# Kernel tuning notes

Hardware: AMD Instinct MI355X
Metric: run time of the kernel (lower is better)

Reference implementation:

```python
import jax, jax.numpy as jnp
import numpy as np

BN_EPS = 0.001
ALPHA = 10.0
WEIGHT_BIT = 8
ACT_BIT = 8
BIAS_BIT = 16


def _ste_round(x, s):
    # straight-through quantize: round(x*s)/s with identity gradient
    return x + jax.lax.stop_gradient(jnp.round(x * s) / s - x)


def _qsym(x, bit):
    # symmetric per-tensor 'scale' quantization
    s = (2.0 ** (bit - 1) - 1.0) / jnp.maximum(jnp.max(jnp.abs(x)), 1e-8)
    return _ste_round(x, s)


def _qrelu(x, alpha, bit):
    # clipped ReLU to [0, alpha] then uniform quantization to 2^bit - 1 levels
    y = jnp.clip(x, 0.0, alpha)
    s = (2.0 ** bit - 1.0) / alpha
    return _ste_round(y, s)


def _folded_qconv(x, w, b, gamma, beta, mean, var, stride, pad):
    # fold BN into conv weights/bias, then quantize weight (8b) and bias (16b)
    sc = gamma / jnp.sqrt(var + BN_EPS)            # [O]
    wf = _qsym(w * sc[:, None, None, None], WEIGHT_BIT)
    bf = _qsym((b - mean) * sc + beta, BIAS_BIT)
    y = jax.lax.conv_general_dilated(
        x, wf, window_strides=stride, padding=[(pad, pad), (pad, pad)],
        dimension_numbers=('NCHW', 'OIHW', 'NCHW'))
    return y + bf[None, :, None, None]


def setup_inputs() -> dict:
    key = jax.random.key(0)
    ks = jax.random.split(key, 20)
    Cin, Cmid, Cout = 256, 128, 512
    d = {'x': jax.random.normal(ks[0], (32, Cin, 56, 56), dtype=jnp.float32)}

    def mk(k0, o, i, kh, kw, tag):
        kk = jax.random.split(k0, 6)
        fan = i * kh * kw
        d['w' + tag] = jax.random.normal(kk[0], (o, i, kh, kw), jnp.float32) * (fan ** -0.5)
        d['b' + tag] = jax.random.normal(kk[1], (o,), jnp.float32) * 0.01
        d['g' + tag] = 1.0 + jax.random.normal(kk[2], (o,), jnp.float32) * 0.1
        d['be' + tag] = jax.random.normal(kk[3], (o,), jnp.float32) * 0.1
        d['m' + tag] = jax.random.normal(kk[4], (o,), jnp.float32) * 0.1
        d['v' + tag] = jax.random.uniform(kk[5], (o,), jnp.float32) + 0.5

    mk(ks[1], Cmid, Cin, 1, 1, '1')
    mk(ks[2], Cmid, Cmid, 3, 3, '2')
    mk(ks[3], Cout, Cmid, 1, 1, '3')
    return d


def reference(x, w1, b1, g1, be1, m1, v1,
              w2, b2, g2, be2, m2, v2,
              w3, b3, g3, be3, m3, v3):
    out = _folded_qconv(x, w1, b1, g1, be1, m1, v1, (1, 1), 0)
    out = _qrelu(out, ALPHA, ACT_BIT)
    out = _folded_qconv(out, w2, b2, g2, be2, m2, v2, (1, 1), 1)
    out = _qrelu(out, ALPHA, ACT_BIT)
    out = _folded_qconv(out, w3, b3, g3, be3, m3, v3, (1, 1), 0)
    return out
```

## Files before the change

### kernel.cpp

```cpp
#include <hip/hip_runtime.h>
#include <math.h>

typedef int v4i  __attribute__((ext_vector_type(4)));
typedef int v16i __attribute__((ext_vector_type(16)));
typedef short v8s __attribute__((ext_vector_type(8)));
typedef float v16f __attribute__((ext_vector_type(16)));

#define N_IMG 32
#define CIN   256
#define CMID  128
#define COUT  512
#define HWP   3136
#define W58   58
#define PLANE_Q 3456
#define CBSTRIDE (PLANE_Q*16)
#define IMGSTRIDE (8*CBSTRIDE)
#define BSROW 248
#define GUARD 16384
#define BN_EPS_F 1e-3f
#define ALPHA_F  10.0f
#define ARELU_S  25.5f

#define OFF_WQ1   0
#define OFF_WF2   32768
#define OFF_WF3   180224
#define OFF_BQ1   245760
#define OFF_BQ2   245888
#define OFF_BQ3   246016
#define OFF_MAX   246528
#define OFF_Q2    246536
#define OFF_Q3    246664
#define OFF_WQ2I  247296
#define OFF_WQ3I  284160
#define OFF_WBF1  300544
#define ACT1Q_GUARD_B 52582400u
#define ACT1Q_B       (ACT1Q_GUARD_B + GUARD)
#define ACT2Q_B       (ACT1Q_B + (unsigned)(N_IMG*IMGSTRIDE) + GUARD)

__device__ __forceinline__ void async16(const char* g, char* l) {
    __builtin_amdgcn_global_load_lds((const __attribute__((address_space(1))) void*)g,
                                     (__attribute__((address_space(3))) void*)l, 16, 0, 0);
}

__device__ __forceinline__ unsigned bf16rne(float f) {
    unsigned u = __float_as_uint(f);
    return (u + 0x7fffu + ((u >> 16) & 1u)) >> 16;
}
__device__ __forceinline__ float bfval(unsigned h) {
    return __uint_as_float(h << 16);
}

__global__ __launch_bounds__(256) void fold_max_kernel(
    const float* __restrict__ w, const float* __restrict__ g,
    const float* __restrict__ v, float* __restrict__ wf,
    unsigned int* __restrict__ maxbits, int inner, int total)
{
    __shared__ float smax[256];
    float m = 0.f;
    for (int i = blockIdx.x * 256 + threadIdx.x; i < total; i += gridDim.x * 256) {
        int o = i / inner;
        float sc = g[o] / sqrtf(v[o] + BN_EPS_F);
        float val = w[i] * sc;
        wf[i] = val;
        m = fmaxf(m, fabsf(val));
    }
    smax[threadIdx.x] = m;
    __syncthreads();
    for (int s = 128; s > 0; s >>= 1) {
        if (threadIdx.x < s) smax[threadIdx.x] = fmaxf(smax[threadIdx.x], smax[threadIdx.x + s]);
        __syncthreads();
    }
    if (threadIdx.x == 0) atomicMax(maxbits, __float_as_uint(smax[0]));
}

__global__ __launch_bounds__(256) void quant_w1_bf16_kernel(
    const float* __restrict__ wf1, const unsigned int* __restrict__ maxbits,
    unsigned short* __restrict__ wbf)
{
    int i = blockIdx.x * 256 + threadIdx.x;
    float s = 127.0f / fmaxf(__uint_as_float(*maxbits), 1e-8f);
    int kb = i >> 10, rem = i & 1023;
    int m = rem >> 3, j = rem & 7;
    int c = kb * 8 + j;
    float k = rintf(wf1[m * CIN + c] * s);
    wbf[i] = (unsigned short)(__float_as_uint(k) >> 16);
}

__global__ __launch_bounds__(256) void quant_w2_kernel(
    const float* __restrict__ wf2, const unsigned int* __restrict__ maxw,
    char* __restrict__ wq2i, int* __restrict__ Q2)
{
    __shared__ int red[256];
    int m = blockIdx.x;
    float s = 127.0f / fmaxf(__uint_as_float(maxw[1]), 1e-8f);
    int sum = 0;
    for (int idx = threadIdx.x; idx < CMID * 9; idx += 256) {
        int c = idx / 9, tap = idx - c * 9;
        int q = (int)rintf(wf2[(size_t)m * (CMID * 9) + idx] * s);
        wq2i[(size_t)tap * (CMID * CMID) + m * CMID + c] = (char)q;
        sum += q;
    }
    red[threadIdx.x] = sum;
    __syncthreads();
    for (int st = 128; st > 0; st >>= 1) {
        if (threadIdx.x < st) red[threadIdx.x] += red[threadIdx.x + st];
        __syncthreads();
    }
    if (threadIdx.x == 0) Q2[m] = red[0];
}

__global__ __launch_bounds__(128) void quant_w3_kernel(
    const float* __restrict__ wf3, const unsigned int* __restrict__ maxw,
    char* __restrict__ wq3i, int* __restrict__ Q3)
{
    __shared__ int red[128];
    int m = blockIdx.x, c = threadIdx.x;
    float s = 127.0f / fmaxf(__uint_as_float(maxw[2]), 1e-8f);
    int q = (int)rintf(wf3[(size_t)m * CMID + c] * s);
    wq3i[(size_t)m * CMID + c] = (char)q;
    red[c] = q;
    __syncthreads();
    for (int st = 64; st > 0; st >>= 1) {
        if (c < st) red[c] += red[c + st];
        __syncthreads();
    }
    if (c == 0) Q3[m] = red[0];
}

__global__ __launch_bounds__(512) void fold_bias_kernel(
    const float* __restrict__ b, const float* __restrict__ g,
    const float* __restrict__ be, const float* __restrict__ m,
    const float* __restrict__ v, float* __restrict__ bq, int n)
{
    __shared__ float red[512];
    int t = threadIdx.x;
    float val = 0.f;
    if (t < n) {
        float sc = g[t] / sqrtf(v[t] + BN_EPS_F);
        val = (b[t] - m[t]) * sc + be[t];
    }
    red[t] = (t < n) ? fabsf(val) : 0.f;
    __syncthreads();
    for (int s = 256; s > 0; s >>= 1) {
        if (t < s) red[t] = fmaxf(red[t], red[t + s]);
        __syncthreads();
    }
    float mx = fmaxf(red[0], 1e-8f);
    float s = 32767.0f / mx;
    if (t < n) bq[t] = rintf(val * s) / s;
}

__global__ __launch_bounds__(256) void conv1_bf16_kernel(
    const float* __restrict__ X, const unsigned short* __restrict__ Wbf,
    const unsigned int* __restrict__ maxw, const float* __restrict__ bq1,
    char* __restrict__ act1q)
{
    __shared__ char lds[65536];
    char* As = lds;
    char* Bh = lds + 16384;
    char* Bm = lds + 32768;
    char* Bl = lds + 49152;
    const int tid = threadIdx.x;
    const int n  = blockIdx.z;
    const int q0 = blockIdx.x * 128;
    const int lane = tid & 63, wid = tid >> 6;
    const int lo = lane & 31, hi = lane >> 5;
    const int wm = wid >> 1, wn = wid & 1;
    const float* Xn = X + (size_t)n * CIN * HWP;

    v16f acc[2][2] = {};

    for (int kc = 0; kc < 4; kc++) {
        __syncthreads();
        const char* wsrc = (const char*)Wbf + kc * 16384;
#pragma unroll
        for (int i = 0; i < 4; i++)
            async16(wsrc + (i * 256 + tid) * 16, As + (i * 256 + tid) * 16);
#pragma unroll
        for (int i = 0; i < 4; i++) {
            int e = i * 256 + tid;
            int kb = e >> 7, qi = e & 127;
            int q = q0 + qi;
            int y = q / W58, xx = q - y * W58;
            int p = (y - 1) * 56 + (xx - 1);
            p = p < 0 ? 0 : (p > HWP - 1 ? HWP - 1 : p);
            const float* src = Xn + (size_t)(kc * 64 + kb * 8) * HWP + p;
            float v[8];
#pragma unroll
            for (int j = 0; j < 8; j++) v[j] = src[j * HWP];
            unsigned ph[4], pm_[4], pl[4];
#pragma unroll
            for (int jj = 0; jj < 4; jj++) {
                float a0 = v[2 * jj], a1 = v[2 * jj + 1];
                unsigned h0 = bf16rne(a0), h1 = bf16rne(a1);
                float r0 = a0 - bfval(h0), r1 = a1 - bfval(h1);
                unsigned m0_ = bf16rne(r0), m1_ = bf16rne(r1);
                float t0 = r0 - bfval(m0_), t1 = r1 - bfval(m1_);
                unsigned l0 = bf16rne(t0), l1 = bf16rne(t1);
                ph[jj]  = h0 | (h1 << 16);
                pm_[jj] = m0_ | (m1_ << 16);
                pl[jj]  = l0 | (l1 << 16);
            }
            int off = (kb * 128 + qi) * 16;
            *(uint4*)(Bh + off) = make_uint4(ph[0], ph[1], ph[2], ph[3]);
            *(uint4*)(Bm + off) = make_uint4(pm_[0], pm_[1], pm_[2], pm_[3]);
            *(uint4*)(Bl + off) = make_uint4(pl[0], pl[1], pl[2], pl[3]);
        }
        __syncthreads();
#pragma unroll
        for (int pass = 0; pass < 3; pass++) {
            const char* Bp = (pass == 0) ? Bh : ((pass == 1) ? Bm : Bl);
#pragma unroll
            for (int ks = 0; ks < 4; ks++) {
                v8s a[2], b[2];
#pragma unroll
                for (int s = 0; s < 2; s++)
                    a[s] = *(const v8s*)(As + ((ks * 2 + hi) * 128 + wm * 64 + s * 32 + lo) * 16);
#pragma unroll
                for (int t = 0; t < 2; t++)
                    b[t] = *(const v8s*)(Bp + ((ks * 2 + hi) * 128 + wn * 64 + t * 32 + lo) * 16);
#pragma unroll
                for (int s = 0; s < 2; s++)
#pragma unroll
                    for (int t = 0; t < 2; t++)
                        acc[s][t] = __builtin_amdgcn_mfma_f32_32x32x16_bf16(a[s], b[t], acc[s][t], 0, 0, 0);
            }
        }
    }

    float inv_s = fmaxf(__uint_as_float(maxw[0]), 1e-8f) / 127.0f;
    __syncthreads();
    char* Cs = lds;
#pragma unroll
    for (int s = 0; s < 2; s++)
#pragma unroll
        for (int t = 0; t < 2; t++) {
            int qloc = wn * 64 + t * 32 + lo;
#pragma unroll
            for (int reg = 0; reg < 16; reg++) {
                int m = wm * 64 + s * 32 + (reg & 3) + 8 * (reg >> 2) + 4 * hi;
                float val = fmaf(acc[s][t][reg], inv_s, bq1[m]);
                val = fminf(fmaxf(val, 0.f), ALPHA_F);
                int k1 = (int)rintf(val * ARELU_S);
                Cs[qloc * 148 + m] = (char)(k1 - 128);
            }
        }
    __syncthreads();
    char* dst = act1q + (size_t)n * IMGSTRIDE + (size_t)q0 * 16;
#pragma unroll
    for (int it = 0; it < 4; it++) {
        int idx = it * 256 + tid;
        int ql = idx >> 3, cb = idx & 7;
        int q = q0 + ql;
        int y = q / W58, xx = q - y * W58;
        if ((unsigned)(y - 1) < 56u && (unsigned)(xx - 1) < 56u) {
            int4 w;
            w.x = *(const int*)(Cs + ql * 148 + cb * 16 + 0);
            w.y = *(const int*)(Cs + ql * 148 + cb * 16 + 4);
            w.z = *(const int*)(Cs + ql * 148 + cb * 16 + 8);
            w.w = *(const int*)(Cs + ql * 148 + cb * 16 + 12);
            *(int4*)(dst + (size_t)cb * CBSTRIDE + ql * 16) = w;
        }
    }
}

__global__ __launch_bounds__(256) void conv2_i8_kernel(
    const char* __restrict__ actq, const char* __restrict__ wq2i,
    const int* __restrict__ Q2, const float* __restrict__ bq2,
    const unsigned int* __restrict__ maxw, char* __restrict__ act2q)
{
    __shared__ char lds[48128];
    char* As2 = lds;
    char* Bs  = lds + 16384;
    const int tid = threadIdx.x;
    const int n  = blockIdx.z;
    const int q0 = blockIdx.x * 128;
    const int lane = tid & 63, wid = tid >> 6;
    const int lo = lane & 31, hi = lane >> 5;
    const int wm = wid >> 1, wn = wid & 1;

    const char* src = actq + (size_t)n * IMGSTRIDE + (long)(q0 - 59) * 16;
#pragma unroll
    for (int cb = 0; cb < 8; cb++) {
        if (tid < 246)
            async16(src + (size_t)cb * CBSTRIDE + tid * 16, Bs + cb * (BSROW * 16) + tid * 16);
    }

    const int sm = tid >> 1, shalf = tid & 1;
    const char* wsrc = wq2i + sm * CMID + shalf * 64;
    char* wdst = As2 + (shalf * 4) * 2048 + sm * 16;
    int4 pre[4];
#pragma unroll
    for (int i = 0; i < 4; i++) pre[i] = *(const int4*)(wsrc + i * 16);

    v16i acc[2][2] = {};

    for (int tap = 0; tap < 9; tap++) {
        __syncthreads();
        int4 cur[4];
#pragma unroll
        for (int i = 0; i < 4; i++) cur[i] = pre[i];
        if (tap < 8) {
            const char* ns = wsrc + (size_t)(tap + 1) * (CMID * CMID);
#pragma unroll
            for (int i = 0; i < 4; i++) pre[i] = *(const int4*)(ns + i * 16);
        }
#pragma unroll
        for (int i = 0; i < 4; i++) *(int4*)(wdst + i * 2048) = cur[i];
        __syncthreads();

        const int tapoff = ((tap / 3) - 1) * W58 + (tap % 3) - 1;
#pragma unroll
        for (int ks = 0; ks < 4; ks++) {
            v4i a[2], b[2];
#pragma unroll
            for (int s = 0; s < 2; s++)
                a[s] = *(const v4i*)(As2 + ((ks * 2 + hi) * 128 + wm * 64 + s * 32 + lo) * 16);
#pragma unroll
            for (int t = 0; t < 2; t++) {
                int ql = 59 + tapoff + wn * 64 + t * 32 + lo;
                b[t] = *(const v4i*)(Bs + ((ks * 2 + hi) * BSROW + ql) * 16);
            }
#pragma unroll
            for (int s = 0; s < 2; s++)
#pragma unroll
                for (int t = 0; t < 2; t++)
                    acc[s][t] = __builtin_amdgcn_mfma_i32_32x32x32_i8(a[s], b[t], acc[s][t], 0, 0, 0);
        }
    }

    float scale = fmaxf(__uint_as_float(maxw[1]), 1e-8f) / (127.0f * ARELU_S);
    __syncthreads();
    char* Cs = lds;
#pragma unroll
    for (int s = 0; s < 2; s++)
#pragma unroll
        for (int t = 0; t < 2; t++) {
            int qloc = wn * 64 + t * 32 + lo;
#pragma unroll
            for (int reg = 0; reg < 16; reg++) {
                int m = wm * 64 + s * 32 + (reg & 3) + 8 * (reg >> 2) + 4 * hi;
                float val = fmaf((float)(acc[s][t][reg] + 128 * Q2[m]), scale, bq2[m]);
                val = fminf(fmaxf(val, 0.f), ALPHA_F);
                int k2 = (int)rintf(val * ARELU_S);
                Cs[qloc * 148 + m] = (char)(k2 - 128);
            }
        }
    __syncthreads();
    char* dst = act2q + (size_t)n * IMGSTRIDE + q0 * 16;
#pragma unroll
    for (int it = 0; it < 4; it++) {
        int idx = it * 256 + tid;
        int q = idx >> 3, cb = idx & 7;
        int4 w;
        w.x = *(const int*)(Cs + q * 148 + cb * 16 + 0);
        w.y = *(const int*)(Cs + q * 148 + cb * 16 + 4);
        w.z = *(const int*)(Cs + q * 148 + cb * 16 + 8);
        w.w = *(const int*)(Cs + q * 148 + cb * 16 + 12);
        *(int4*)(dst + (size_t)cb * CBSTRIDE + q * 16) = w;
    }
}

__global__ __launch_bounds__(256) void conv3_i8_kernel(
    const char* __restrict__ act2q, const char* __restrict__ wq3i,
    const int* __restrict__ Q3, const float* __restrict__ bq3,
    const unsigned int* __restrict__ maxw, float* __restrict__ out)
{
    __shared__ char lds[32768];
    char* As2 = lds;
    char* Bs  = lds + 16384;
    const int tid = threadIdx.x;
    const int n  = blockIdx.z;
    const int q0 = blockIdx.x * 128;
    const int m0 = blockIdx.y * 128;
    const int lane = tid & 63, wid = tid >> 6;
    const int lo = lane & 31, hi = lane >> 5;
    const int wm = wid >> 1, wn = wid & 1;

    const char* bsrc = act2q + (size_t)n * IMGSTRIDE + q0 * 16;
#pragma unroll
    for (int i = 0; i < 4; i++) {
        int cb = i * 2 + (tid >> 7), row = tid & 127;
        async16(bsrc + (size_t)cb * CBSTRIDE + row * 16, Bs + cb * 2048 + row * 16);
    }

    const int sm = tid >> 1, shalf = tid & 1;
    const char* wsrc = wq3i + (size_t)(m0 + sm) * CMID + shalf * 64;
    char* wdst = As2 + (shalf * 4) * 2048 + sm * 16;
    int4 w[4];
#pragma unroll
    for (int i = 0; i < 4; i++) w[i] = *(const int4*)(wsrc + i * 16);
#pragma unroll
    for (int i = 0; i < 4; i++) *(int4*)(wdst + i * 2048) = w[i];
    __syncthreads();

    v16i acc[2][2] = {};
#pragma unroll
    for (int ks = 0; ks < 4; ks++) {
        v4i a[2], b[2];
#pragma unroll
        for (int s = 0; s < 2; s++)
            a[s] = *(const v4i*)(As2 + ((ks * 2 + hi) * 128 + wm * 64 + s * 32 + lo) * 16);
#pragma unroll
        for (int t = 0; t < 2; t++)
            b[t] = *(const v4i*)(Bs + ((ks * 2 + hi) * 128 + wn * 64 + t * 32 + lo) * 16);
#pragma unroll
        for (int s = 0; s < 2; s++)
#pragma unroll
            for (int t = 0; t < 2; t++)
                acc[s][t] = __builtin_amdgcn_mfma_i32_32x32x32_i8(a[s], b[t], acc[s][t], 0, 0, 0);
    }

    float scale = fmaxf(__uint_as_float(maxw[2]), 1e-8f) / (127.0f * ARELU_S);
#pragma unroll
    for (int s = 0; s < 2; s++)
#pragma unroll
        for (int t = 0; t < 2; t++) {
            int q = q0 + wn * 64 + t * 32 + lo;
            int y = q / W58, x = q - y * W58;
            if ((unsigned)(y - 1) < 56u && (unsigned)(x - 1) < 56u) {
                int p = (y - 1) * 56 + (x - 1);
                float* op = out + (size_t)n * COUT * HWP + p;
#pragma unroll
                for (int reg = 0; reg < 16; reg++) {
                    int m = m0 + wm * 64 + s * 32 + (reg & 3) + 8 * (reg >> 2) + 4 * hi;
                    op[(size_t)m * HWP] = fmaf((float)(acc[s][t][reg] + 128 * Q3[m]), scale, bq3[m]);
                }
            }
        }
}

extern "C" void kernel_launch(void* const* d_in, const int* in_sizes, int n_in,
                              void* d_out, int out_size, void* d_ws, size_t ws_size,
                              hipStream_t stream) {
    const float* x   = (const float*)d_in[0];
    const float* w1  = (const float*)d_in[1];
    const float* b1  = (const float*)d_in[2];
    const float* g1  = (const float*)d_in[3];
    const float* be1 = (const float*)d_in[4];
    const float* m1  = (const float*)d_in[5];
    const float* v1  = (const float*)d_in[6];
    const float* w2  = (const float*)d_in[7];
    const float* b2  = (const float*)d_in[8];
    const float* g2  = (const float*)d_in[9];
    const float* be2 = (const float*)d_in[10];
    const float* m2  = (const float*)d_in[11];
    const float* v2  = (const float*)d_in[12];
    const float* w3  = (const float*)d_in[13];
    const float* b3  = (const float*)d_in[14];
    const float* g3  = (const float*)d_in[15];
    const float* be3 = (const float*)d_in[16];
    const float* m3  = (const float*)d_in[17];
    const float* v3  = (const float*)d_in[18];

    float* ws  = (float*)d_ws;
    unsigned char* wsb = (unsigned char*)d_ws;
    float* wq1 = ws + OFF_WQ1;
    float* wf2 = ws + OFF_WF2;
    float* wf3 = ws + OFF_WF3;
    float* bq1 = ws + OFF_BQ1;
    float* bq2 = ws + OFF_BQ2;
    float* bq3 = ws + OFF_BQ3;
    unsigned int* maxw = (unsigned int*)(ws + OFF_MAX);
    int* Q2 = (int*)(ws + OFF_Q2);
    int* Q3 = (int*)(ws + OFF_Q3);
    char* wq2i = (char*)(ws + OFF_WQ2I);
    char* wq3i = (char*)(ws + OFF_WQ3I);
    unsigned short* wbf = (unsigned short*)(ws + OFF_WBF1);
    char* act1q = (char*)(wsb + ACT1Q_B);
    char* act2q = (char*)(wsb + ACT2Q_B);
    float* out  = (float*)d_out;

    hipMemsetAsync(maxw, 0, 12, stream);
    hipMemsetAsync(wsb + ACT1Q_GUARD_B, 0x80, (size_t)GUARD + (size_t)N_IMG * IMGSTRIDE + GUARD, stream);

    fold_max_kernel<<<128, 256, 0, stream>>>(w1, g1, v1, wq1, maxw + 0, CIN,      CMID * CIN);
    fold_max_kernel<<<256, 256, 0, stream>>>(w2, g2, v2, wf2, maxw + 1, CMID * 9, CMID * CMID * 9);
    fold_max_kernel<<<256, 256, 0, stream>>>(w3, g3, v3, wf3, maxw + 2, CMID,     COUT * CMID);

    quant_w1_bf16_kernel<<<128, 256, 0, stream>>>(wq1, maxw + 0, wbf);
    quant_w2_kernel<<<CMID, 256, 0, stream>>>(wf2, maxw, wq2i, Q2);
    quant_w3_kernel<<<COUT, 128, 0, stream>>>(wf3, maxw, wq3i, Q3);

    fold_bias_kernel<<<1, 512, 0, stream>>>(b1, g1, be1, m1, v1, bq1, CMID);
    fold_bias_kernel<<<1, 512, 0, stream>>>(b2, g2, be2, m2, v2, bq2, CMID);
    fold_bias_kernel<<<1, 512, 0, stream>>>(b3, g3, be3, m3, v3, bq3, COUT);

    conv1_bf16_kernel<<<dim3(26, 1, 32), 256, 0, stream>>>(x, wbf, maxw, bq1, act1q);
    conv2_i8_kernel<<<dim3(27, 1, 32), 256, 0, stream>>>(act1q, wq2i, Q2, bq2, maxw, act2q);
    conv3_i8_kernel<<<dim3(27, 4, 32), 256, 0, stream>>>(act2q, wq3i, Q3, bq3, maxw, out);
}
```

Before: 521.6 us.

## Fuse prep kernels, read weights from global, vectorize conv1 input loads

Merges the nine weight/bias fold and quantize launches into two kernels. Drops the large border memset by having conv1 write the 0x80 padding value itself, with an extra grid column covering the tail. The conv kernels now read weight fragments straight from global memory in a pre-tiled layout instead of staging them in LDS, which shrinks LDS use. conv1 loads four pixels per thread with float4 when they are contiguous, and splits bf16 by truncation instead of round-to-nearest. These cut launch overhead, memset bandwidth and LDS traffic, but make weight reads depend on cache hits and change the rounding of the split.

```diff
diff --git a/kernel.cpp b/kernel.cpp
--- a/kernel.cpp
+++ b/kernel.cpp
@@ -42,112 +42,109 @@
                                      (__attribute__((address_space(3))) void*)l, 16, 0, 0);
 }
 
-__device__ __forceinline__ unsigned bf16rne(float f) {
-    unsigned u = __float_as_uint(f);
-    return (u + 0x7fffu + ((u >> 16) & 1u)) >> 16;
-}
-__device__ __forceinline__ float bfval(unsigned h) {
-    return __uint_as_float(h << 16);
-}
-
-__global__ __launch_bounds__(256) void fold_max_kernel(
-    const float* __restrict__ w, const float* __restrict__ g,
-    const float* __restrict__ v, float* __restrict__ wf,
-    unsigned int* __restrict__ maxbits, int inner, int total)
+__global__ __launch_bounds__(256) void fold_all_kernel(
+    const float* __restrict__ w1, const float* __restrict__ g1, const float* __restrict__ v1,
+    const float* __restrict__ w2, const float* __restrict__ g2, const float* __restrict__ v2,
+    const float* __restrict__ w3, const float* __restrict__ g3, const float* __restrict__ v3,
+    const float* __restrict__ b1, const float* __restrict__ be1, const float* __restrict__ m1,
+    const float* __restrict__ b2, const float* __restrict__ be2, const float* __restrict__ m2,
+    const float* __restrict__ b3, const float* __restrict__ be3, const float* __restrict__ m3,
+    float* __restrict__ wq1, float* __restrict__ wf2, float* __restrict__ wf3,
+    float* __restrict__ bq1, float* __restrict__ bq2, float* __restrict__ bq3,
+    unsigned int* __restrict__ maxw)
 {
-    __shared__ float smax[256];
-    float m = 0.f;
-    for (int i = blockIdx.x * 256 + threadIdx.x; i < total; i += gridDim.x * 256) {
+    __shared__ float red[256];
+    const int b = blockIdx.x, t = threadIdx.x;
+    if (b < 960) {
+        const float *w, *g, *v; float* wf; int inner; unsigned int* mslot; int i;
+        if (b < 128)      { w = w1; g = g1; v = v1; wf = wq1; inner = CIN;      mslot = maxw + 0; i = b * 256 + t; }
+        else if (b < 704) { w = w2; g = g2; v = v2; wf = wf2; inner = CMID * 9; mslot = maxw + 1; i = (b - 128) * 256 + t; }
+        else              { w = w3; g = g3; v = v3; wf = wf3; inner = CMID;     mslot = maxw + 2; i = (b - 704) * 256 + t; }
         int o = i / inner;
         float sc = g[o] / sqrtf(v[o] + BN_EPS_F);
         float val = w[i] * sc;
         wf[i] = val;
-        m = fmaxf(m, fabsf(val));
-    }
-    smax[threadIdx.x] = m;
-    __syncthreads();
-    for (int s = 128; s > 0; s >>= 1) {
-        if (threadIdx.x < s) smax[threadIdx.x] = fmaxf(smax[threadIdx.x], smax[threadIdx.x + s]);
-        __syncthreads();
-    }
-    if (threadIdx.x == 0) atomicMax(maxbits, __float_as_uint(smax[0]));
-}
-
-__global__ __launch_bounds__(256) void quant_w1_bf16_kernel(
-    const float* __restrict__ wf1, const unsigned int* __restrict__ maxbits,
-    unsigned short* __restrict__ wbf)
-{
-    int i = blockIdx.x * 256 + threadIdx.x;
-    float s = 127.0f / fmaxf(__uint_as_float(*maxbits), 1e-8f);
-    int kb = i >> 10, rem = i & 1023;
-    int m = rem >> 3, j = rem & 7;
-    int c = kb * 8 + j;
-    float k = rintf(wf1[m * CIN + c] * s);
-    wbf[i] = (unsigned short)(__float_as_uint(k) >> 16);
-}
-
-__global__ __launch_bounds__(256) void quant_w2_kernel(
-    const float* __restrict__ wf2, const unsigned int* __restrict__ maxw,
-    char* __restrict__ wq2i, int* __restrict__ Q2)
+        red[t] = fabsf(val);
+        __syncthreads();
+        for (int s = 128; s > 0; s >>= 1) {
+            if (t < s) red[t] = fmaxf(red[t], red[t + s]);
+            __syncthreads();
+        }
+        if (t == 0) atomicMax(mslot, __float_as_uint(red[0]));
+    } else {
+        const float *bb, *gg, *bebe, *mm, *vv; float* bq; int nn;
+        if (b == 960)      { bb = b1; gg = g1; bebe = be1; mm = m1; vv = v1; bq = bq1; nn = CMID; }
+        else if (b == 961) { bb = b2; gg = g2; bebe = be2; mm = m2; vv = v2; bq = bq2; nn = CMID; }
+        else               { bb = b3; gg = g3; bebe = be3; mm = m3; vv = v3; bq = bq3; nn = COUT; }
+        float val0 = 0.f, val1 = 0.f;
+        if (t < nn) {
+            float sc = gg[t] / sqrtf(vv[t] + BN_EPS_F);
+            val0 = (bb[t] - mm[t]) * sc + bebe[t];
+        }
+        int t2 = t + 256;
+        if (t2 < nn) {
+            float sc = gg[t2] / sqrtf(vv[t2] + BN_EPS_F);
+            val1 = (bb[t2] - mm[t2]) * sc + bebe[t2];
+        }
+        red[t] = fmaxf(fabsf(val0), fabsf(val1));
+        __syncthreads();
+        for (int s = 128; s > 0; s >>= 1) {
+            if (t < s) red[t] = fmaxf(red[t], red[t + s]);
+            __syncthreads();
+        }
+        float mx = fmaxf(red[0], 1e-8f);
+        float s = 32767.0f / mx;
+        if (t < nn)  bq[t]  = rintf(val0 * s) / s;
+        if (t2 < nn) bq[t2] = rintf(val1 * s) / s;
+    }
+}
+
+__global__ __launch_bounds__(256) void quant_all_kernel(
+    const float* __restrict__ wq1f, const float* __restrict__ wf2, const float* __restrict__ wf3,
+    const unsigned int* __restrict__ maxw,
+    unsigned short* __restrict__ wbf, char* __restrict__ wq2i, char* __restrict__ wq3i,
+    int* __restrict__ Q2, int* __restrict__ Q3)
 {
     __shared__ int red[256];
-    int m = blockIdx.x;
-    float s = 127.0f / fmaxf(__uint_as_float(maxw[1]), 1e-8f);
-    int sum = 0;
-    for (int idx = threadIdx.x; idx < CMID * 9; idx += 256) {
-        int c = idx / 9, tap = idx - c * 9;
-        int q = (int)rintf(wf2[(size_t)m * (CMID * 9) + idx] * s);
-        wq2i[(size_t)tap * (CMID * CMID) + m * CMID + c] = (char)q;
-        sum += q;
-    }
-    red[threadIdx.x] = sum;
-    __syncthreads();
-    for (int st = 128; st > 0; st >>= 1) {
-        if (threadIdx.x < st) red[threadIdx.x] += red[threadIdx.x + st];
-        __syncthreads();
-    }
-    if (threadIdx.x == 0) Q2[m] = red[0];
-}
-
-__global__ __launch_bounds__(128) void quant_w3_kernel(
-    const float* __restrict__ wf3, const unsigned int* __restrict__ maxw,
-    char* __restrict__ wq3i, int* __restrict__ Q3)
-{
-    __shared__ int red[128];
-    int m = blockIdx.x, c = threadIdx.x;
-    float s = 127.0f / fmaxf(__uint_as_float(maxw[2]), 1e-8f);
-    int q = (int)rintf(wf3[(size_t)m * CMID + c] * s);
-    wq3i[(size_t)m * CMID + c] = (char)q;
-    red[c] = q;
-    __syncthreads();
-    for (int st = 64; st > 0; st >>= 1) {
-        if (c < st) red[c] += red[c + st];
-        __syncthreads();
-    }
-    if (c == 0) Q3[m] = red[0];
-}
-
-__global__ __launch_bounds__(512) void fold_bias_kernel(
-    const float* __restrict__ b, const float* __restrict__ g,
-    const float* __restrict__ be, const float* __restrict__ m,
-    const float* __restrict__ v, float* __restrict__ bq, int n)
-{
-    __shared__ float red[512];
-    int t = threadIdx.x;
-    float val = 0.f;
-    if (t < n) {
-        float sc = g[t] / sqrtf(v[t] + BN_EPS_F);
-        val = (b[t] - m[t]) * sc + be[t];
-    }
-    red[t] = (t < n) ? fabsf(val) : 0.f;
-    __syncthreads();
-    for (int s = 256; s > 0; s >>= 1) {
-        if (t < s) red[t] = fmaxf(red[t], red[t + s]);
-        __syncthreads();
-    }
-    float mx = fmaxf(red[0], 1e-8f);
-    float s = 32767.0f / mx;
-    if (t < n) bq[t] = rintf(val * s) / s;
+    const int b = blockIdx.x, t = threadIdx.x;
+    if (b < 128) {
+        int i = b * 256 + t;
+        float s = 127.0f / fmaxf(__uint_as_float(maxw[0]), 1e-8f);
+        int kb = i >> 10, rem = i & 1023;
+        int m = rem >> 3, j = rem & 7;
+        int c = kb * 8 + j;
+        float k = rintf(wq1f[m * CIN + c] * s);
+        wbf[i] = (unsigned short)(__float_as_uint(k) >> 16);
+    } else if (b < 256) {
+        int m = b - 128;
+        float s = 127.0f / fmaxf(__uint_as_float(maxw[1]), 1e-8f);
+        int sum = 0;
+        for (int idx = t; idx < CMID * 9; idx += 256) {
+            int c = idx / 9, tap = idx - c * 9;
+            int q = (int)rintf(wf2[(size_t)m * (CMID * 9) + idx] * s);
+            wq2i[(size_t)tap * 16384 + (c >> 4) * 2048 + m * 16 + (c & 15)] = (char)q;
+            sum += q;
+        }
+        red[t] = sum;
+        __syncthreads();
+        for (int st = 128; st > 0; st >>= 1) {
+            if (t < st) red[t] += red[t + st];
+            __syncthreads();
+        }
+        if (t == 0) Q2[m] = red[0];
+    } else {
+        int m = (b - 256) * 2 + (t >> 7), c = t & 127;
+        float s = 127.0f / fmaxf(__uint_as_float(maxw[2]), 1e-8f);
+        int q = (int)rintf(wf3[(size_t)m * CMID + c] * s);
+        wq3i[(size_t)(c >> 4) * 8192 + m * 16 + (c & 15)] = (char)q;
+        red[t] = q;
+        __syncthreads();
+        for (int st = 64; st > 0; st >>= 1) {
+            if ((t & 127) < st) red[t] += red[t + st];
+            __syncthreads();
+        }
+        if ((t & 127) == 0) Q3[m] = red[t];
+    }
 }
 
 __global__ __launch_bounds__(256) void conv1_bf16_kernel(
@@ -155,11 +152,10 @@
     const unsigned int* __restrict__ maxw, const float* __restrict__ bq1,
     char* __restrict__ act1q)
 {
-    __shared__ char lds[65536];
-    char* As = lds;
-    char* Bh = lds + 16384;
-    char* Bm = lds + 32768;
-    char* Bl = lds + 49152;
+    __shared__ char lds[49152];
+    char* Bh = lds;
+    char* Bm = lds + 16384;
+    char* Bl = lds + 32768;
     const int tid = threadIdx.x;
     const int n  = blockIdx.z;
     const int q0 = blockIdx.x * 128;
@@ -168,54 +164,71 @@
     const int wm = wid >> 1, wn = wid & 1;
     const float* Xn = X + (size_t)n * CIN * HWP;
 
+    const int skb = tid >> 5, sqq = tid & 31;
+    const int qq0 = q0 + sqq * 4;
+    int p_[4];
+#pragma unroll
+    for (int e = 0; e < 4; e++) {
+        int q = qq0 + e;
+        int y = q / W58, xx = q - y * W58;
+        int p = (y - 1) * 56 + (xx - 1);
+        p_[e] = p < 0 ? 0 : (p > HWP - 1 ? HWP - 1 : p);
+    }
+    const bool fast = (p_[1] == p_[0] + 1) && (p_[2] == p_[0] + 2) && (p_[3] == p_[0] + 3);
+
     v16f acc[2][2] = {};
 
     for (int kc = 0; kc < 4; kc++) {
         __syncthreads();
-        const char* wsrc = (const char*)Wbf + kc * 16384;
-#pragma unroll
-        for (int i = 0; i < 4; i++)
-            async16(wsrc + (i * 256 + tid) * 16, As + (i * 256 + tid) * 16);
-#pragma unroll
-        for (int i = 0; i < 4; i++) {
-            int e = i * 256 + tid;
-            int kb = e >> 7, qi = e & 127;
-            int q = q0 + qi;
-            int y = q / W58, xx = q - y * W58;
-            int p = (y - 1) * 56 + (xx - 1);
-            p = p < 0 ? 0 : (p > HWP - 1 ? HWP - 1 : p);
-            const float* src = Xn + (size_t)(kc * 64 + kb * 8) * HWP + p;
-            float v[8];
-#pragma unroll
-            for (int j = 0; j < 8; j++) v[j] = src[j * HWP];
+        const float* chbase = Xn + (size_t)(kc * 64 + skb * 8) * HWP;
+        float v[8][4];
+#pragma unroll
+        for (int j = 0; j < 8; j++) {
+            const float* cp = chbase + (size_t)j * HWP;
+            if (fast) {
+                float4 f = *(const float4*)(cp + p_[0]);
+                v[j][0] = f.x; v[j][1] = f.y; v[j][2] = f.z; v[j][3] = f.w;
+            } else {
+#pragma unroll
+                for (int e = 0; e < 4; e++) v[j][e] = cp[p_[e]];
+            }
+        }
+#pragma unroll
+        for (int e = 0; e < 4; e++) {
             unsigned ph[4], pm_[4], pl[4];
 #pragma unroll
             for (int jj = 0; jj < 4; jj++) {
-                float a0 = v[2 * jj], a1 = v[2 * jj + 1];
-                unsigned h0 = bf16rne(a0), h1 = bf16rne(a1);
-                float r0 = a0 - bfval(h0), r1 = a1 - bfval(h1);
-                unsigned m0_ = bf16rne(r0), m1_ = bf16rne(r1);
-                float t0 = r0 - bfval(m0_), t1 = r1 - bfval(m1_);
-                unsigned l0 = bf16rne(t0), l1 = bf16rne(t1);
-                ph[jj]  = h0 | (h1 << 16);
-                pm_[jj] = m0_ | (m1_ << 16);
-                pl[jj]  = l0 | (l1 << 16);
-            }
-            int off = (kb * 128 + qi) * 16;
+                float a0 = v[2 * jj][e], a1 = v[2 * jj + 1][e];
+                unsigned u0 = __float_as_uint(a0), u1 = __float_as_uint(a1);
+                unsigned h0 = u0 & 0xFFFF0000u, h1 = u1 & 0xFFFF0000u;
+                float r0 = a0 - __uint_as_float(h0), r1 = a1 - __uint_as_float(h1);
+                unsigned w0 = __float_as_uint(r0) & 0xFFFF0000u;
+                unsigned w1 = __float_as_uint(r1) & 0xFFFF0000u;
+                float s0 = r0 - __uint_as_float(w0), s1 = r1 - __uint_as_float(w1);
+                unsigned l0 = __float_as_uint(s0) & 0xFFFF0000u;
+                unsigned l1 = __float_as_uint(s1) & 0xFFFF0000u;
+                ph[jj]  = (h0 >> 16) | h1;
+                pm_[jj] = (w0 >> 16) | w1;
+                pl[jj]  = (l0 >> 16) | l1;
+            }
+            int off = (skb * 128 + sqq * 4 + e) * 16;
             *(uint4*)(Bh + off) = make_uint4(ph[0], ph[1], ph[2], ph[3]);
             *(uint4*)(Bm + off) = make_uint4(pm_[0], pm_[1], pm_[2], pm_[3]);
             *(uint4*)(Bl + off) = make_uint4(pl[0], pl[1], pl[2], pl[3]);
         }
         __syncthreads();
-#pragma unroll
-        for (int pass = 0; pass < 3; pass++) {
-            const char* Bp = (pass == 0) ? Bh : ((pass == 1) ? Bm : Bl);
-#pragma unroll
-            for (int ks = 0; ks < 4; ks++) {
-                v8s a[2], b[2];
-#pragma unroll
-                for (int s = 0; s < 2; s++)
-                    a[s] = *(const v8s*)(As + ((ks * 2 + hi) * 128 + wm * 64 + s * 32 + lo) * 16);
+
+        const char* wbase = (const char*)Wbf + kc * 16384;
+#pragma unroll
+        for (int ks = 0; ks < 4; ks++) {
+            v8s a[2];
+#pragma unroll
+            for (int s = 0; s < 2; s++)
+                a[s] = *(const v8s*)(wbase + (((ks * 2 + hi) * 128) + wm * 64 + s * 32 + lo) * 16);
+#pragma unroll
+            for (int pass = 0; pass < 3; pass++) {
+                const char* Bp = (pass == 0) ? Bh : ((pass == 1) ? Bm : Bl);
+                v8s b[2];
 #pragma unroll
                 for (int t = 0; t < 2; t++)
                     b[t] = *(const v8s*)(Bp + ((ks * 2 + hi) * 128 + wn * 64 + t * 32 + lo) * 16);
@@ -253,14 +266,16 @@
         int ql = idx >> 3, cb = idx & 7;
         int q = q0 + ql;
         int y = q / W58, xx = q - y * W58;
+        int4 w;
         if ((unsigned)(y - 1) < 56u && (unsigned)(xx - 1) < 56u) {
-            int4 w;
             w.x = *(const int*)(Cs + ql * 148 + cb * 16 + 0);
             w.y = *(const int*)(Cs + ql * 148 + cb * 16 + 4);
             w.z = *(const int*)(Cs + ql * 148 + cb * 16 + 8);
             w.w = *(const int*)(Cs + ql * 148 + cb * 16 + 12);
-            *(int4*)(dst + (size_t)cb * CBSTRIDE + ql * 16) = w;
-        }
+        } else {
+            w = make_int4(0x80808080, 0x80808080, 0x80808080, 0x80808080);
+        }
+        *(int4*)(dst + (size_t)cb * CBSTRIDE + ql * 16) = w;
     }
 }
 
@@ -269,9 +284,8 @@
     const int* __restrict__ Q2, const float* __restrict__ bq2,
     const unsigned int* __restrict__ maxw, char* __restrict__ act2q)
 {
-    __shared__ char lds[48128];
-    char* As2 = lds;
-    char* Bs  = lds + 16384;
+    __shared__ char lds[31744];
+    char* Bs = lds;
     const int tid = threadIdx.x;
     const int n  = blockIdx.z;
     const int q0 = blockIdx.x * 128;
@@ -285,37 +299,18 @@
         if (tid < 246)
             async16(src + (size_t)cb * CBSTRIDE + tid * 16, Bs + cb * (BSROW * 16) + tid * 16);
     }
-
-    const int sm = tid >> 1, shalf = tid & 1;
-    const char* wsrc = wq2i + sm * CMID + shalf * 64;
-    char* wdst = As2 + (shalf * 4) * 2048 + sm * 16;
-    int4 pre[4];
-#pragma unroll
-    for (int i = 0; i < 4; i++) pre[i] = *(const int4*)(wsrc + i * 16);
+    __syncthreads();
 
     v16i acc[2][2] = {};
-
     for (int tap = 0; tap < 9; tap++) {
-        __syncthreads();
-        int4 cur[4];
-#pragma unroll
-        for (int i = 0; i < 4; i++) cur[i] = pre[i];
-        if (tap < 8) {
-            const char* ns = wsrc + (size_t)(tap + 1) * (CMID * CMID);
-#pragma unroll
-            for (int i = 0; i < 4; i++) pre[i] = *(const int4*)(ns + i * 16);
-        }
-#pragma unroll
-        for (int i = 0; i < 4; i++) *(int4*)(wdst + i * 2048) = cur[i];
-        __syncthreads();
-
+        const char* wt = wq2i + (size_t)tap * 16384;
         const int tapoff = ((tap / 3) - 1) * W58 + (tap % 3) - 1;
 #pragma unroll
         for (int ks = 0; ks < 4; ks++) {
             v4i a[2], b[2];
 #pragma unroll
             for (int s = 0; s < 2; s++)
-                a[s] = *(const v4i*)(As2 + ((ks * 2 + hi) * 128 + wm * 64 + s * 32 + lo) * 16);
+                a[s] = *(const v4i*)(wt + (ks * 2 + hi) * 2048 + (wm * 64 + s * 32 + lo) * 16);
 #pragma unroll
             for (int t = 0; t < 2; t++) {
                 int ql = 59 + tapoff + wn * 64 + t * 32 + lo;
@@ -366,9 +361,8 @@
     const int* __restrict__ Q3, const float* __restrict__ bq3,
     const unsigned int* __restrict__ maxw, float* __restrict__ out)
 {
-    __shared__ char lds[32768];
-    char* As2 = lds;
-    char* Bs  = lds + 16384;
+    __shared__ char lds[16384];
+    char* Bs = lds;
     const int tid = threadIdx.x;
     const int n  = blockIdx.z;
     const int q0 = blockIdx.x * 128;
@@ -383,15 +377,6 @@
         int cb = i * 2 + (tid >> 7), row = tid & 127;
         async16(bsrc + (size_t)cb * CBSTRIDE + row * 16, Bs + cb * 2048 + row * 16);
     }
-
-    const int sm = tid >> 1, shalf = tid & 1;
-    const char* wsrc = wq3i + (size_t)(m0 + sm) * CMID + shalf * 64;
-    char* wdst = As2 + (shalf * 4) * 2048 + sm * 16;
-    int4 w[4];
-#pragma unroll
-    for (int i = 0; i < 4; i++) w[i] = *(const int4*)(wsrc + i * 16);
-#pragma unroll
-    for (int i = 0; i < 4; i++) *(int4*)(wdst + i * 2048) = w[i];
     __syncthreads();
 
     v16i acc[2][2] = {};
@@ -400,7 +385,7 @@
         v4i a[2], b[2];
 #pragma unroll
         for (int s = 0; s < 2; s++)
-            a[s] = *(const v4i*)(As2 + ((ks * 2 + hi) * 128 + wm * 64 + s * 32 + lo) * 16);
+            a[s] = *(const v4i*)(wq3i + (ks * 2 + hi) * 8192 + (m0 + wm * 64 + s * 32 + lo) * 16);
 #pragma unroll
         for (int t = 0; t < 2; t++)
             b[t] = *(const v4i*)(Bs + ((ks * 2 + hi) * 128 + wn * 64 + t * 32 + lo) * 16);
@@ -472,21 +457,15 @@
     float* out  = (float*)d_out;
 
     hipMemsetAsync(maxw, 0, 12, stream);
-    hipMemsetAsync(wsb + ACT1Q_GUARD_B, 0x80, (size_t)GUARD + (size_t)N_IMG * IMGSTRIDE + GUARD, stream);
-
-    fold_max_kernel<<<128, 256, 0, stream>>>(w1, g1, v1, wq1, maxw + 0, CIN,      CMID * CIN);
-    fold_max_kernel<<<256, 256, 0, stream>>>(w2, g2, v2, wf2, maxw + 1, CMID * 9, CMID * CMID * 9);
-    fold_max_kernel<<<256, 256, 0, stream>>>(w3, g3, v3, wf3, maxw + 2, CMID,     COUT * CMID);
-
-    quant_w1_bf16_kernel<<<128, 256, 0, stream>>>(wq1, maxw + 0, wbf);
-    quant_w2_kernel<<<CMID, 256, 0, stream>>>(wf2, maxw, wq2i, Q2);
-    quant_w3_kernel<<<COUT, 128, 0, stream>>>(wf3, maxw, wq3i, Q3);
-
-    fold_bias_kernel<<<1, 512, 0, stream>>>(b1, g1, be1, m1, v1, bq1, CMID);
-    fold_bias_kernel<<<1, 512, 0, stream>>>(b2, g2, be2, m2, v2, bq2, CMID);
-    fold_bias_kernel<<<1, 512, 0, stream>>>(b3, g3, be3, m3, v3, bq3, COUT);
-
-    conv1_bf16_kernel<<<dim3(26, 1, 32), 256, 0, stream>>>(x, wbf, maxw, bq1, act1q);
+
+    fold_all_kernel<<<963, 256, 0, stream>>>(
+        w1, g1, v1, w2, g2, v2, w3, g3, v3,
+        b1, be1, m1, b2, be2, m2, b3, be3, m3,
+        wq1, wf2, wf3, bq1, bq2, bq3, maxw);
+
+    quant_all_kernel<<<512, 256, 0, stream>>>(wq1, wf2, wf3, maxw, wbf, wq2i, wq3i, Q2, Q3);
+
+    conv1_bf16_kernel<<<dim3(27, 1, 32), 256, 0, stream>>>(x, wbf, maxw, bq1, act1q);
     conv2_i8_kernel<<<dim3(27, 1, 32), 256, 0, stream>>>(act1q, wq2i, Q2, bq2, maxw, act2q);
     conv3_i8_kernel<<<dim3(27, 4, 32), 256, 0, stream>>>(act2q, wq3i, Q3, bq3, maxw, out);
 }
```

Measured after the change: 455.1 us. -12.8%, faster.
